# Performance work log

Measured on AMD Instinct MI355X. Metric: run time of the kernel, lower is better.

The kernel has to match this reference:

```python
import jax, jax.numpy as jnp
import numpy as np

D = 1024
H = 16
HD = D // H
T = 2048
B = 2
EPS = 1e-7

def setup_inputs() -> dict:
    key = jax.random.key(0)
    ks = jax.random.split(key, 16)
    s = 0.02
    return {
        "x":  jax.random.normal(ks[0], (B, T, D), jnp.float32),
        "Wq": jax.random.normal(ks[1], (D, D), jnp.float32) * s,
        "bq": jnp.zeros((D,), jnp.float32),
        "Wk": jax.random.normal(ks[2], (D, D), jnp.float32) * s,
        "bk": jnp.zeros((D,), jnp.float32),
        "Wv": jax.random.normal(ks[3], (D, D), jnp.float32) * s,
        "bv": jnp.zeros((D,), jnp.float32),
        "Wo": jax.random.normal(ks[4], (D, D), jnp.float32) * s,
        "bo": jnp.zeros((D,), jnp.float32),
        "W1": jax.random.normal(ks[5], (D, 4 * D), jnp.float32) * s,
        "b1": jnp.zeros((4 * D,), jnp.float32),
        "W2": jax.random.normal(ks[6], (4 * D, D), jnp.float32) * s,
        "b2": jnp.zeros((D,), jnp.float32),
        "g1": jnp.ones((D,), jnp.float32),
        "be1": jnp.zeros((D,), jnp.float32),
        "g2": jnp.ones((D,), jnp.float32),
        "be2": jnp.zeros((D,), jnp.float32),
    }

def layer_norm(x, gamma, beta):
    mu = jnp.mean(x, axis=-1, keepdims=True)
    var = jnp.mean(jnp.square(x - mu), axis=-1, keepdims=True)  # biased var
    return (x - mu) / jnp.sqrt(var + EPS) * gamma + beta

def attention(x, Wq, bq, Wk, bk, Wv, bv, Wo, bo):
    b, t, d = x.shape
    q = (x @ Wq + bq).reshape(b, t, H, HD).transpose(0, 2, 1, 3)  # [B,H,T,HD]
    k = (x @ Wk + bk).reshape(b, t, H, HD).transpose(0, 2, 1, 3)
    v = (x @ Wv + bv).reshape(b, t, H, HD).transpose(0, 2, 1, 3)
    scores = jnp.einsum("bhqd,bhkd->bhqk", q, k) / np.sqrt(HD).astype(np.float32)
    causal = jnp.tril(jnp.ones((t, t), bool))
    scores = jnp.where(causal, scores, -jnp.inf)
    attn = jax.nn.softmax(scores, axis=-1)
    out = jnp.einsum("bhqk,bhkd->bhqd", attn, v)
    out = out.transpose(0, 2, 1, 3).reshape(b, t, d)
    return out @ Wo + bo

def reference(x, Wq, bq, Wk, bk, Wv, bv, Wo, bo, W1, b1, W2, b2, g1, be1, g2, be2):
    x = x + attention(layer_norm(x, g1, be1), Wq, bq, Wk, bk, Wv, bv, Wo, bo)
    h = layer_norm(x, g2, be2)
    x = x + (jax.nn.relu(h @ W1 + b1) @ W2 + b2)
    return x
```

## Files before the change

kernel.cpp:

```cpp
#include <hip/hip_runtime.h>
#include <hip/hip_bf16.h>

#define Dm 1024
#define Hn 16
#define HDm 64
#define Tm 2048
#define Bm 2
#define MR (Bm*Tm)
#define SQK 3072

typedef __attribute__((ext_vector_type(8))) short bfrag8;
typedef __attribute__((ext_vector_type(4))) float floatx4;

__device__ __forceinline__ float bf2f(ushort u){
  union { unsigned int i; float f; } c; c.i = ((unsigned int)u)<<16; return c.f;
}
__device__ __forceinline__ ushort f2bf(float f){
  unsigned int u = __float_as_uint(f);
  u += 0x7fffu + ((u>>16)&1u);
  return (ushort)(u>>16);
}
__device__ __forceinline__ void gl2lds16(const ushort* g, ushort* l){
  __builtin_amdgcn_global_load_lds(
    (const __attribute__((address_space(1))) unsigned int*)g,
    (__attribute__((address_space(3))) unsigned int*)l,
    16, 0, 0);
}
__device__ __forceinline__ int is_f32(const unsigned int* g1w){
  return *g1w == 0x3F800000u;
}

#define POFF0 (1ul*524288)
#define POFF1 (9ul*524288)
#define POFF2 (25ul*524288)
#define POFF3 (73ul*524288)

__global__ __launch_bounds__(256) void prep_vec(const void* bq, const void* bk, const void* bv,
                                                const void* bo, const void* b1, const void* b2,
                                                const void* g1, const void* be1,
                                                const void* g2, const void* be2,
                                                float* __restrict__ dst){
  int i = blockIdx.x*256 + threadIdx.x;
  if (i >= 13312) return;
  int f = is_f32((const unsigned int*)g1);
  const void* src; int off;
  if      (i < 1024)  { src = bq;  off = i; }
  else if (i < 2048)  { src = bk;  off = i-1024; }
  else if (i < 3072)  { src = bv;  off = i-2048; }
  else if (i < 4096)  { src = bo;  off = i-3072; }
  else if (i < 8192)  { src = b1;  off = i-4096; }
  else if (i < 9216)  { src = b2;  off = i-8192; }
  else if (i < 10240) { src = g1;  off = i-9216; }
  else if (i < 11264) { src = be1; off = i-10240; }
  else if (i < 12288) { src = g2;  off = i-11264; }
  else                { src = be2; off = i-12288; }
  dst[i] = f ? ((const float*)src)[off] : bf2f(((const ushort*)src)[off]);
}

__device__ __forceinline__ void transpose_body(const void* src, ushort* dst,
                                               int K, int N, int f32){
  __shared__ ushort s[32][33];
  int bx = blockIdx.x, by = blockIdx.y;
  int tx = threadIdx.x, ty = threadIdx.y;
#pragma unroll
  for(int r=0;r<4;r++){
    size_t gi = (size_t)(by*32+ty+8*r)*N + bx*32+tx;
    s[ty+8*r][tx] = f32 ? f2bf(((const float*)src)[gi]) : ((const ushort*)src)[gi];
  }
  __syncthreads();
#pragma unroll
  for(int r=0;r<4;r++)
    dst[(size_t)(bx*32+ty+8*r)*K + by*32+tx] = s[tx][ty+8*r];
}
__global__ __launch_bounds__(256) void transpose_cast(const void* __restrict__ src,
                                                      ushort* __restrict__ dst,
                                                      int K, int N, const unsigned int* g1w){
  transpose_body(src, dst, K, N, is_f32(g1w));
}
__global__ __launch_bounds__(256) void transpose_qkvo(const void* Wq, const void* Wk,
                                                      const void* Wv, const void* Wo,
                                                      ushort* __restrict__ Wqkvt,
                                                      ushort* __restrict__ Wot,
                                                      const unsigned int* g1w){
  int z = blockIdx.z;
  const void* src = (z==0)?Wq:(z==1)?Wk:(z==2)?Wv:Wo;
  ushort* dst = (z<3) ? (Wqkvt + (size_t)z*1024*1024) : Wot;
  transpose_body(src, dst, 1024, 1024, is_f32(g1w));
}

__global__ __launch_bounds__(256) void vtrans(const ushort* __restrict__ qkv,
                                              ushort* __restrict__ vt){
  __shared__ ushort s[32][33];
  int bhz = blockIdx.z;
  int bx = blockIdx.x;
  int by = blockIdx.y;
  int tx = threadIdx.x, ty = threadIdx.y;
  int b = bhz>>4, h = bhz&15;
  const ushort* src = qkv + (size_t)b*Tm*SQK + 2048 + h*64;
#pragma unroll
  for(int r=0;r<4;r++)
    s[ty+8*r][tx] = src[(size_t)(bx*32+ty+8*r)*SQK + by*32+tx];
  __syncthreads();
  ushort* dst = vt + (size_t)bhz*HDm*Tm;
#pragma unroll
  for(int r=0;r<4;r++)
    dst[(size_t)(by*32+ty+8*r)*Tm + bx*32+tx] = s[tx][ty+8*r];
}

template<int MODE>
__global__ __launch_bounds__(256) void ln_kernel(const void* __restrict__ xin,
                                                 const float* __restrict__ g,
                                                 const float* __restrict__ be,
                                                 ushort* __restrict__ out,
                                                 const unsigned int* g1w){
  int row = blockIdx.x;
  int tid = threadIdx.x;
  size_t base = (size_t)row*Dm + tid*4;
  float v[4];
  bool f32in = (MODE==1) || (MODE==0 && is_f32(g1w));
  if (f32in){
    const float4 t = *(const float4*)((const float*)xin + base);
    v[0]=t.x; v[1]=t.y; v[2]=t.z; v[3]=t.w;
  } else {
    ushort4 t = *(const ushort4*)((const ushort*)xin + base);
    v[0]=bf2f(t.x); v[1]=bf2f(t.y); v[2]=bf2f(t.z); v[3]=bf2f(t.w);
  }
  float s  = v[0]+v[1]+v[2]+v[3];
  float s2 = v[0]*v[0]+v[1]*v[1]+v[2]*v[2]+v[3]*v[3];
#pragma unroll
  for(int o=1;o<64;o<<=1){
    s  += __shfl_xor(s,  o, 64);
    s2 += __shfl_xor(s2, o, 64);
  }
  __shared__ float red[8];
  int wv = tid>>6;
  if ((tid&63)==0){ red[wv]=s; red[wv+4]=s2; }
  __syncthreads();
  s  = red[0]+red[1]+red[2]+red[3];
  s2 = red[4]+red[5]+red[6]+red[7];
  float mu  = s  * (1.0f/Dm);
  float var = s2 * (1.0f/Dm) - mu*mu;
  float rstd = rsqrtf(var + 1e-7f);
  float4 gg = *(const float4*)(g  + tid*4);
  float4 bb = *(const float4*)(be + tid*4);
  ushort4 o4;
  o4.x = f2bf((v[0]-mu)*rstd*gg.x+bb.x);
  o4.y = f2bf((v[1]-mu)*rstd*gg.y+bb.y);
  o4.z = f2bf((v[2]-mu)*rstd*gg.z+bb.z);
  o4.w = f2bf((v[3]-mu)*rstd*gg.w+bb.w);
  *(ushort4*)(out + base) = o4;
}

#define BKt 64
enum { E_BF16=0, E_RELU=1, E_OPROJ=2, E_FINALB=3, E_PARTB=4, E_PARTB4=5 };

template<int EPI>
__global__ __launch_bounds__(512,2) void gemm256(const ushort* __restrict__ A, int lda,
                                                 const ushort* __restrict__ Bt, int ldb,
                                                 const float* __restrict__ bias,
                                                 void* __restrict__ Cout, int ldc,
                                                 int Ki,
                                                 const unsigned int* g1w){
  __shared__ ushort lds[65536];
  int tid = threadIdx.x;
  int lin = blockIdx.x;
  int xcd = lin&7, pos = lin>>3;
  int bm, bn, zid = 0;
  if (EPI==E_BF16){        bm=(xcd&3)*4+(pos&3);  bn=(xcd>>2)*6+(pos>>2); }
  else if (EPI==E_RELU){   bm=(xcd&3)*4+(pos&3);  bn=(xcd>>2)*8+(pos>>2); }
  else if (EPI==E_PARTB4){ zid=xcd>>1; bm=(xcd&1)*8+(pos>>2); bn=pos&3; }
  else {                   zid=xcd&1;  bm=(xcd>>1)*4+(pos>>2); bn=pos&3; }
  int wv = tid>>6, lane = tid&63;
  int quad = lane>>4, l16 = lane&15;
  int wm = (wv>>2)*128, wn = (wv&3)*64;
  int rl = lane>>3;
  int cs = ((lane&7)^rl)*8;
  const ushort* Aptr = A  + (size_t)bm*256*lda + (size_t)zid*Ki;
  const ushort* Bptr = Bt + (size_t)bn*256*ldb + (size_t)zid*Ki;
  floatx4 acc[8][4] = {};
  bfrag8 afr[4][2], bfr[4][2];
  const int NI = Ki>>7;

  auto STG = [&](ushort* dst, const ushort* g, int ld){
    gl2lds16(&g[(size_t)(wv*16+rl)*ld + cs],   dst + (wv*16)*64);
    gl2lds16(&g[(size_t)(wv*16+8+rl)*ld + cs], dst + (wv*16+8)*64);
  };
  auto LD8 = [&](const ushort* base, int r, int G)->bfrag8{
    return *(const bfrag8*)&base[r*64 + ((G ^ (r&7))<<3)];
  };
#define BAR256 __builtin_amdgcn_s_barrier()
#define LGKM0  do{ asm volatile("s_waitcnt lgkmcnt(0)" ::: "memory"); __builtin_amdgcn_sched_barrier(0);}while(0)
#define MM256(a_,b_,c_) c_ = __builtin_amdgcn_mfma_f32_16x16x32_bf16(a_,b_,c_,0,0,0)

  STG(lds+32768,      Bptr,                    ldb);
  STG(lds+32768+8192, Bptr+(size_t)128*ldb,    ldb);
  STG(lds,            Aptr,                    lda);
  STG(lds+8192,       Aptr+(size_t)128*lda,    lda);
  STG(lds+49152,      Bptr+64,                 ldb);
  STG(lds+49152+8192, Bptr+(size_t)128*ldb+64, ldb);
  STG(lds+16384,      Aptr+64,                 lda);
  asm volatile("s_waitcnt vmcnt(6)" ::: "memory");
  BAR256;

  for(int i=0;i<NI;i++){
    bool nl = (i < NI-1);
    int kc = i*128;
#pragma unroll
    for(int m=0;m<4;m++){ int r=wm+m*16+l16;
      afr[m][0]=LD8(lds, r, quad);  afr[m][1]=LD8(lds, r, 4|quad); }
#pragma unroll
    for(int j=0;j<4;j++){ int r=wn+j*16+l16;
      bfr[j][0]=LD8(lds+32768, r, quad); bfr[j][1]=LD8(lds+32768, r, 4|quad); }
    STG(lds+16384+8192, Aptr+(size_t)128*lda + kc+64, lda);
    BAR256; LGKM0;
    __builtin_amdgcn_s_setprio(1);
#pragma unroll
    for(int m=0;m<4;m++)
#pragma unroll
      for(int j=0;j<2;j++){ MM256(afr[m][0],bfr[j][0],acc[m][j]); MM256(afr[m][1],bfr[j][1],acc[m][j]); }
    __builtin_amdgcn_s_setprio(0);
    BAR256;
    if(nl) STG(lds+32768, Bptr + kc+128, ldb);
    BAR256;
    __builtin_amdgcn_s_setprio(1);
#pragma unroll
    for(int m=0;m<4;m++)
#pragma unroll
      for(int j=2;j<4;j++){ MM256(afr[m][0],bfr[j][0],acc[m][j]); MM256(afr[m][1],bfr[j][1],acc[m][j]); }
    __builtin_amdgcn_s_setprio(0);
    BAR256;
#pragma unroll
    for(int m=0;m<4;m++){ int r=wm+(4+m)*16+l16;
      afr[m][0]=LD8(lds, r, quad);  afr[m][1]=LD8(lds, r, 4|quad); }
    if(nl) STG(lds+32768+8192, Bptr+(size_t)128*ldb + kc+128, ldb);
    BAR256; LGKM0;
    __builtin_amdgcn_s_setprio(1);
#pragma unroll
    for(int m=0;m<4;m++)
#pragma unroll
      for(int j=2;j<4;j++){ MM256(afr[m][0],bfr[j][0],acc[4+m][j]); MM256(afr[m][1],bfr[j][1],acc[4+m][j]); }
    __builtin_amdgcn_s_setprio(0);
    BAR256;
    if(nl) STG(lds, Aptr + kc+128, lda);
    BAR256;
    __builtin_amdgcn_s_setprio(1);
#pragma unroll
    for(int m=0;m<4;m++)
#pragma unroll
      for(int j=0;j<2;j++){ MM256(afr[m][0],bfr[j][0],acc[4+m][j]); MM256(afr[m][1],bfr[j][1],acc[4+m][j]); }
    __builtin_amdgcn_s_setprio(0);
    if(nl) asm volatile("s_waitcnt vmcnt(6)" ::: "memory");
    else   asm volatile("s_waitcnt vmcnt(0)" ::: "memory");
    BAR256;
#pragma unroll
    for(int m=0;m<4;m++){ int r=wm+m*16+l16;
      afr[m][0]=LD8(lds+16384, r, quad);  afr[m][1]=LD8(lds+16384, r, 4|quad); }
#pragma unroll
    for(int j=0;j<4;j++){ int r=wn+j*16+l16;
      bfr[j][0]=LD8(lds+49152, r, quad); bfr[j][1]=LD8(lds+49152, r, 4|quad); }
    if(nl) STG(lds+8192, Aptr+(size_t)128*lda + kc+128, lda);
    BAR256; LGKM0;
    __builtin_amdgcn_s_setprio(1);
#pragma unroll
    for(int m=0;m<4;m++)
#pragma unroll
      for(int j=0;j<2;j++){ MM256(afr[m][0],bfr[j][0],acc[m][j]); MM256(afr[m][1],bfr[j][1],acc[m][j]); }
    __builtin_amdgcn_s_setprio(0);
    BAR256;
    if(nl) STG(lds+49152, Bptr + kc+192, ldb);
    BAR256;
    __builtin_amdgcn_s_setprio(1);
#pragma unroll
    for(int m=0;m<4;m++)
#pragma unroll
      for(int j=2;j<4;j++){ MM256(afr[m][0],bfr[j][0],acc[m][j]); MM256(afr[m][1],bfr[j][1],acc[m][j]); }
    __builtin_amdgcn_s_setprio(0);
    BAR256;
#pragma unroll
    for(int m=0;m<4;m++){ int r=wm+(4+m)*16+l16;
      afr[m][0]=LD8(lds+16384, r, quad);  afr[m][1]=LD8(lds+16384, r, 4|quad); }
    if(nl) STG(lds+49152+8192, Bptr+(size_t)128*ldb + kc+192, ldb);
    BAR256; LGKM0;
    __builtin_amdgcn_s_setprio(1);
#pragma unroll
    for(int m=0;m<4;m++)
#pragma unroll
      for(int j=2;j<4;j++){ MM256(afr[m][0],bfr[j][0],acc[4+m][j]); MM256(afr[m][1],bfr[j][1],acc[4+m][j]); }
    __builtin_amdgcn_s_setprio(0);
    BAR256;
    if(nl) STG(lds+16384, Aptr + kc+192, lda);
    BAR256;
    __builtin_amdgcn_s_setprio(1);
#pragma unroll
    for(int m=0;m<4;m++)
#pragma unroll
      for(int j=0;j<2;j++){ MM256(afr[m][0],bfr[j][0],acc[4+m][j]); MM256(afr[m][1],bfr[j][1],acc[4+m][j]); }
    __builtin_amdgcn_s_setprio(0);
    if(nl){ asm volatile("s_waitcnt vmcnt(6)" ::: "memory"); }
    BAR256;
  }

  ushort* part = (ushort*)Cout;
  if (EPI==E_PARTB)  part += (size_t)zid*MR*1024;
  if (EPI==E_PARTB4) part += (zid==0?POFF0 : zid==1?POFF1 : zid==2?POFF2 : POFF3);
#pragma unroll
  for(int i2=0;i2<8;i2++){
    int gr = bm*256 + wm + i2*16 + quad*4;
#pragma unroll
    for(int j=0;j<4;j++){
      int gc = bn*256 + wn + j*16 + l16;
      float bb = (EPI==E_PARTB || EPI==E_PARTB4) ? 0.0f : bias[gc];
#pragma unroll
      for(int rg=0; rg<4; rg++){
        size_t idx = (size_t)(gr+rg)*ldc + gc;
        float val = acc[i2][j][rg] + bb;
        if (EPI==E_RELU) part[idx] = f2bf(val>0.0f?val:0.0f);
        else             part[idx] = f2bf(val);
      }
    }
  }
#undef BAR256
#undef LGKM0
#undef MM256
}

__global__ __launch_bounds__(256) void ffn2_reduce(const ushort* __restrict__ p0,
                                                   const ushort* __restrict__ p1,
                                                   const float* __restrict__ bias,
                                                   const ushort* __restrict__ resid,
                                                   void* __restrict__ out,
                                                   const unsigned int* g1w){
  int e = (blockIdx.x*256 + threadIdx.x)*4;
  ushort4 a = *(const ushort4*)&p0[e];
  ushort4 b = *(const ushort4*)&p1[e];
  ushort4 r = *(const ushort4*)&resid[e];
  float4 bb = *(const float4*)&bias[e & 1023];
  float v0 = bf2f(a.x)+bf2f(b.x)+bb.x+bf2f(r.x);
  float v1 = bf2f(a.y)+bf2f(b.y)+bb.y+bf2f(r.y);
  float v2 = bf2f(a.z)+bf2f(b.z)+bb.z+bf2f(r.z);
  float v3 = bf2f(a.w)+bf2f(b.w)+bb.w+bf2f(r.w);
  if (is_f32(g1w)){
    float4 o = {v0,v1,v2,v3};
    *(float4*)((float*)out + e) = o;
  } else {
    ushort4 o = {f2bf(v0),f2bf(v1),f2bf(v2),f2bf(v3)};
    *(ushort4*)((ushort*)out + e) = o;
  }
}

__global__ __launch_bounds__(256) void ffn2_reduce4(const ushort* __restrict__ pb,
                                                    const float* __restrict__ bias,
                                                    const ushort* __restrict__ resid,
                                                    void* __restrict__ out,
                                                    const unsigned int* g1w){
  int e = (blockIdx.x*256 + threadIdx.x)*4;
  ushort4 a = *(const ushort4*)&pb[POFF0 + e];
  ushort4 b = *(const ushort4*)&pb[POFF1 + e];
  ushort4 c = *(const ushort4*)&pb[POFF2 + e];
  ushort4 d = *(const ushort4*)&pb[POFF3 + e];
  ushort4 r = *(const ushort4*)&resid[e];
  float4 bb = *(const float4*)&bias[e & 1023];
  float v0 = bf2f(a.x)+bf2f(b.x)+bf2f(c.x)+bf2f(d.x)+bb.x+bf2f(r.x);
  float v1 = bf2f(a.y)+bf2f(b.y)+bf2f(c.y)+bf2f(d.y)+bb.y+bf2f(r.y);
  float v2 = bf2f(a.z)+bf2f(b.z)+bf2f(c.z)+bf2f(d.z)+bb.z+bf2f(r.z);
  float v3 = bf2f(a.w)+bf2f(b.w)+bf2f(c.w)+bf2f(d.w)+bb.w+bf2f(r.w);
  if (is_f32(g1w)){
    float4 o = {v0,v1,v2,v3};
    *(float4*)((float*)out + e) = o;
  } else {
    ushort4 o = {f2bf(v0),f2bf(v1),f2bf(v2),f2bf(v3)};
    *(ushort4*)((ushort*)out + e) = o;
  }
}

template<int EPI>
__global__ __launch_bounds__(128) void gemm64_bt(const ushort* __restrict__ A, int lda,
                                                 const ushort* __restrict__ Bt, int ldb,
                                                 const float* __restrict__ bias,
                                                 const void*   __restrict__ resid,
                                                 void* __restrict__ Cout, int ldc,
                                                 int Ki,
                                                 const unsigned int* g1w){
  __shared__ ushort As[64*BKt];
  __shared__ ushort Bs[64*BKt];
  int tid = threadIdx.x;
  int id = blockIdx.x;
  int xcd = id&7, sdec = id>>3;
  int bn = sdec&15, bm = (sdec>>4)*8 + xcd;
  int wv = tid>>6, lane = tid&63;
  int quad = lane>>4, l16 = lane&15;
  int wm = wv*32;
  floatx4 acc[2][4] = {};
  const ushort* Aptr = A  + (size_t)bm*64*lda;
  const ushort* Bptr = Bt + (size_t)bn*64*ldb;
  int rl = lane>>3;
  int cs = ((lane&7) ^ rl)*8;

  for(int k0=0; k0<Ki; k0+=BKt){
    __syncthreads();
#pragma unroll
    for(int c=0;c<4;c++){
      gl2lds16(&Aptr[(size_t)(wv*32 + c*8 + rl)*lda + k0 + cs], &As[(wv*32 + c*8)*BKt]);
      gl2lds16(&Bptr[(size_t)(wv*32 + c*8 + rl)*ldb + k0 + cs], &Bs[(wv*32 + c*8)*BKt]);
    }
    __syncthreads();
#pragma unroll
    for(int f=0;f<2;f++){
      int sw = (((f<<2)|quad) ^ (l16&7))*8;
      bfrag8 a[2], b[4];
#pragma unroll
      for(int i=0;i<2;i++) a[i] = *(const bfrag8*)&As[(wm+i*16+l16)*BKt + sw];
#pragma unroll
      for(int j=0;j<4;j++) b[j] = *(const bfrag8*)&Bs[(j*16+l16)*BKt + sw];
#pragma unroll
      for(int i=0;i<2;i++)
#pragma unroll
        for(int j=0;j<4;j++)
          acc[i][j] = __builtin_amdgcn_mfma_f32_16x16x32_bf16(a[i], b[j], acc[i][j], 0,0,0);
    }
  }

  int f32 = is_f32(g1w);
#pragma unroll
  for(int i=0;i<2;i++){
    int gr = bm*64 + wm + i*16 + quad*4;
#pragma unroll
    for(int j=0;j<4;j++){
      int gc = bn*64 + j*16 + l16;
      float bb = bias[gc];
#pragma unroll
      for(int rg=0; rg<4; rg++){
        size_t idx = (size_t)(gr+rg)*ldc + gc;
        float val = acc[i][j][rg] + bb;
        if (EPI==E_OPROJ){
          float r = f32 ? ((const float*)resid)[idx] : bf2f(((const ushort*)resid)[idx]);
          ((ushort*)Cout)[idx] = f2bf(val + r);
        } else {
          float r = bf2f(((const ushort*)resid)[idx]);
          if (f32) ((float*)Cout)[idx] = val + r;
          else     ((ushort*)Cout)[idx] = f2bf(val + r);
        }
      }
    }
  }
}

#define PSTR2 132

__global__ __launch_bounds__(256) void attn_mfma(const ushort* __restrict__ qkv,
                                                 const ushort* __restrict__ vt,
                                                 ushort* __restrict__ out){
  __shared__ ushort Ks[128*64];
  __shared__ ushort Vs[64*128];
  __shared__ ushort Ps[64*PSTR2];
  int id = blockIdx.x;
  int xcd = id&7, sdec = id>>3;
  int qt = 31 - (sdec&31);
  int hb = sdec>>5;
  int h = xcd + 8*(hb&1), b = hb>>1;
  int tid = threadIdx.x;
  int wv = tid>>6, lane = tid&63;
  int quad = lane>>4, l16 = lane&15;
  const ushort* qbase = qkv + (size_t)b*Tm*SQK + h*HDm;
  const ushort* kbase = qbase + Dm;
  const ushort* vtb   = vt + (size_t)(b*Hn+h)*HDm*Tm;
  size_t obase = (size_t)b*Tm*Dm + (size_t)h*HDm;
  int rl = lane>>3;
  int cs = ((lane&7) ^ rl)*8;
  int vrow = lane>>4;
  int vg = lane&15;

  int qrow = qt*64 + wv*16 + l16;
  bfrag8 aq[2];
#pragma unroll
  for(int f=0;f<2;f++){
    bfrag8 raw = *(const bfrag8*)&qbase[(size_t)qrow*SQK + f*32 + quad*8];
#pragma unroll
    for(int e=0;e<8;e++) aq[f][e] = (short)f2bf(bf2f((ushort)raw[e])*0.125f);
  }

  floatx4 oacc[4] = {};
  float lacc = 0.0f;
  int qglob = qt*64 + wv*16 + l16;
  int nr = (qt+2)>>1;

  for(int r=0; r<nr; r++){
    __syncthreads();
#pragma unroll
    for(int c=0;c<4;c++){
      int kr0 = wv*32 + c*8;
      gl2lds16(&kbase[(size_t)(r*128 + kr0 + rl)*SQK + cs], &Ks[kr0*64]);
      int d0 = wv*16 + c*4;
      int drow = d0 + vrow;
      int gg = vg ^ (drow&7);
      gl2lds16(&vtb[(size_t)drow*Tm + r*128 + gg*8], &Vs[d0*128]);
    }
    __syncthreads();

    floatx4 s[8];
#pragma unroll
    for(int j=0;j<8;j++){
      int kr = j*16 + l16;
      int k7 = kr & 7;
      bfrag8 k0 = *(const bfrag8*)&Ks[kr*64 + ((quad     ^ k7)*8)];
      bfrag8 k1 = *(const bfrag8*)&Ks[kr*64 + (((4|quad) ^ k7)*8)];
      floatx4 z = {0.0f,0.0f,0.0f,0.0f};
      z = __builtin_amdgcn_mfma_f32_16x16x32_bf16(k0, aq[0], z, 0,0,0);
      z = __builtin_amdgcn_mfma_f32_16x16x32_bf16(k1, aq[1], z, 0,0,0);
      s[j] = z;
    }
    if (2*r+1 >= qt){
#pragma unroll
      for(int j=0;j<8;j++){
        int gk0 = r*128 + j*16 + quad*4;
#pragma unroll
        for(int rg=0;rg<4;rg++)
          if (gk0 + rg > qglob) s[j][rg] = -1.0e30f;
      }
    }

#pragma unroll
    for(int j=0;j<8;j++){
      float p0 = __expf(s[j][0]);
      float p1 = __expf(s[j][1]);
      float p2 = __expf(s[j][2]);
      float p3 = __expf(s[j][3]);
      lacc += (p0+p1)+(p2+p3);
      unsigned w0, w1;
      asm("v_cvt_pk_bf16_f32 %0, %1, %2" : "=v"(w0) : "v"(p0), "v"(p1));
      asm("v_cvt_pk_bf16_f32 %0, %1, %2" : "=v"(w1) : "v"(p2), "v"(p3));
      uint2 ww; ww.x = w0; ww.y = w1;
      *(uint2*)&Ps[(wv*16 + l16)*PSTR2 + j*16 + quad*4] = ww;
    }

    bfrag8 ap[4];
#pragma unroll
    for(int c=0;c<4;c++)
      ap[c] = *(const bfrag8*)&Ps[(wv*16 + l16)*PSTR2 + c*32 + quad*8];

#pragma unroll
    for(int j=0;j<4;j++){
      int dr = j*16 + l16;
      int d7 = dr & 7;
#pragma unroll
      for(int c=0;c<4;c++){
        bfrag8 bv = *(const bfrag8*)&Vs[dr*128 + (((c*4+quad) ^ d7)*8)];
        oacc[j] = __builtin_amdgcn_mfma_f32_16x16x32_bf16(ap[c], bv, oacc[j], 0,0,0);
      }
    }
  }

  lacc += __shfl_xor(lacc, 16, 64);
  lacc += __shfl_xor(lacc, 32, 64);
  float inv[4];
#pragma unroll
  for(int rg=0;rg<4;rg++){
    float den = __shfl(lacc, quad*4 + rg, 64);
    inv[rg] = 1.0f / den;
  }

#pragma unroll
  for(int j=0;j<4;j++)
#pragma unroll
    for(int rg=0;rg<4;rg++){
      int t = qt*64 + wv*16 + quad*4 + rg;
      out[obase + (size_t)t*Dm + j*16 + l16] = f2bf(oacc[j][rg] * inv[rg]);
    }
}

extern "C" void kernel_launch(void* const* d_in, const int* in_sizes, int n_in,
                              void* d_out, int out_size, void* d_ws, size_t ws_size,
                              hipStream_t stream) {
  const void* x   = d_in[0];
  const void* Wq  = d_in[1];
  const void* bq  = d_in[2];
  const void* Wk  = d_in[3];
  const void* bk  = d_in[4];
  const void* Wv  = d_in[5];
  const void* bv  = d_in[6];
  const void* Wo  = d_in[7];
  const void* bo  = d_in[8];
  const void* W1  = d_in[9];
  const void* b1  = d_in[10];
  const void* W2  = d_in[11];
  const void* b2  = d_in[12];
  const void* g1  = d_in[13];
  const void* be1 = d_in[14];
  const void* g2  = d_in[15];
  const void* be2 = d_in[16];
  const unsigned int* g1w = (const unsigned int*)g1;

  char* ws = (char*)d_ws;
  const size_t MB = 1024*1024;
  float*  biasf = (float*)(ws + 65536);
  ushort* Wqkvt = (ushort*)(ws + 1*MB);
  ushort* Wot   = (ushort*)(ws + 7*MB);
  ushort* W1t   = (ushort*)(ws + 9*MB);
  ushort* W2t   = (ushort*)(ws + 17*MB);
  ushort* p0    = (ushort*)(ws + 1*MB);
  ushort* p1    = (ushort*)(ws + 9*MB);
  ushort* ln1   = (ushort*)(ws + 25*MB);
  ushort* vtb   = (ushort*)(ws + 25*MB);
  ushort* h2    = (ushort*)(ws + 25*MB);
  ushort* qkv   = (ushort*)(ws + 33*MB);
  ushort* atb   = (ushort*)(ws + 57*MB);
  ushort* x1b   = (ushort*)(ws + 65*MB);
  ushort* h1    = (ushort*)(ws + 33*MB);

  prep_vec<<<52, 256, 0, stream>>>(bq,bk,bv,bo,b1,b2,g1,be1,g2,be2, biasf);

  dim3 tb(32,8);
  transpose_qkvo<<<dim3(32,32,4), tb, 0, stream>>>(Wq, Wk, Wv, Wo, Wqkvt, Wot, g1w);
  transpose_cast<<<dim3(128,32), tb, 0, stream>>>(W1, W1t, 1024, 4096, g1w);
  transpose_cast<<<dim3(32,128), tb, 0, stream>>>(W2, W2t, 4096, 1024, g1w);

  ln_kernel<0><<<MR, 256, 0, stream>>>(x, biasf+9216, biasf+10240, ln1, g1w);

  gemm256<E_BF16><<<192, 512, 0, stream>>>(ln1, 1024, Wqkvt, 1024, biasf, qkv, SQK, 1024, g1w);

  vtrans<<<dim3(64,2,32), tb, 0, stream>>>(qkv, vtb);

  attn_mfma<<<1024, 256, 0, stream>>>(qkv, vtb, atb);

  gemm64_bt<E_OPROJ><<<1024, 128, 0, stream>>>(atb, 1024, Wot, 1024, biasf+3072, x, x1b, 1024, 1024, g1w);

  ln_kernel<2><<<MR, 256, 0, stream>>>(x1b, biasf+11264, biasf+12288, h2, g1w);

  gemm256<E_RELU><<<256, 512, 0, stream>>>(h2, 1024, W1t, 1024, biasf+4096, h1, 4096, 1024, g1w);

  if (ws_size >= 82*MB){
    gemm256<E_PARTB4><<<256, 512, 0, stream>>>(h1, 4096, W2t, 4096, nullptr, d_ws, 1024, 1024, g1w);
    ffn2_reduce4<<<4096, 256, 0, stream>>>((const ushort*)d_ws, biasf+8192, x1b, d_out, g1w);
  } else {
    gemm256<E_PARTB><<<128, 512, 0, stream>>>(h1, 4096, W2t, 4096, nullptr, p0, 1024, 2048, g1w);
    ffn2_reduce<<<4096, 256, 0, stream>>>(p0, p1, biasf+8192, x1b, d_out, g1w);
  }
}
```

Before: 339.8 us.

## Halve attention block to two waves, each processing two 16-row query groups

The attention kernel now runs 128 threads per block instead of 256. Each wave handles 32 query rows as two 16-row groups, so every K and V fragment read from LDS feeds two MFMAs. Each wave issues twice as many global-to-LDS loads per tile, and the P buffer stride changes from 132 to 136. The aim is fewer LDS reads per MFMA, at the cost of more registers per wave and fewer waves per block to hide latency.

```diff
diff --git a/kernel.cpp b/kernel.cpp
--- a/kernel.cpp
+++ b/kernel.cpp
@@ -445,9 +445,9 @@
   }
 }
 
-#define PSTR2 132
-
-__global__ __launch_bounds__(256) void attn_mfma(const ushort* __restrict__ qkv,
+#define PSTR2 136
+
+__global__ __launch_bounds__(128) void attn_mfma(const ushort* __restrict__ qkv,
                                                  const ushort* __restrict__ vt,
                                                  ushort* __restrict__ out){
   __shared__ ushort Ks[128*64];
@@ -470,73 +470,87 @@
   int vrow = lane>>4;
   int vg = lane&15;
 
-  int qrow = qt*64 + wv*16 + l16;
-  bfrag8 aq[2];
-#pragma unroll
-  for(int f=0;f<2;f++){
-    bfrag8 raw = *(const bfrag8*)&qbase[(size_t)qrow*SQK + f*32 + quad*8];
-#pragma unroll
-    for(int e=0;e<8;e++) aq[f][e] = (short)f2bf(bf2f((ushort)raw[e])*0.125f);
-  }
-
-  floatx4 oacc[4] = {};
-  float lacc = 0.0f;
-  int qglob = qt*64 + wv*16 + l16;
+  bfrag8 aq[2][2];
+#pragma unroll
+  for(int g=0;g<2;g++){
+    int qrow = qt*64 + wv*32 + g*16 + l16;
+#pragma unroll
+    for(int f=0;f<2;f++){
+      bfrag8 raw = *(const bfrag8*)&qbase[(size_t)qrow*SQK + f*32 + quad*8];
+#pragma unroll
+      for(int e=0;e<8;e++) aq[g][f][e] = (short)f2bf(bf2f((ushort)raw[e])*0.125f);
+    }
+  }
+
+  floatx4 oacc[2][4] = {};
+  float lacc[2] = {0.0f, 0.0f};
   int nr = (qt+2)>>1;
 
   for(int r=0; r<nr; r++){
     __syncthreads();
 #pragma unroll
-    for(int c=0;c<4;c++){
-      int kr0 = wv*32 + c*8;
+    for(int c=0;c<8;c++){
+      int kr0 = wv*64 + c*8;
       gl2lds16(&kbase[(size_t)(r*128 + kr0 + rl)*SQK + cs], &Ks[kr0*64]);
-      int d0 = wv*16 + c*4;
+      int d0 = wv*32 + c*4;
       int drow = d0 + vrow;
       int gg = vg ^ (drow&7);
       gl2lds16(&vtb[(size_t)drow*Tm + r*128 + gg*8], &Vs[d0*128]);
     }
     __syncthreads();
 
-    floatx4 s[8];
+    floatx4 s[2][8];
 #pragma unroll
     for(int j=0;j<8;j++){
       int kr = j*16 + l16;
       int k7 = kr & 7;
       bfrag8 k0 = *(const bfrag8*)&Ks[kr*64 + ((quad     ^ k7)*8)];
       bfrag8 k1 = *(const bfrag8*)&Ks[kr*64 + (((4|quad) ^ k7)*8)];
-      floatx4 z = {0.0f,0.0f,0.0f,0.0f};
-      z = __builtin_amdgcn_mfma_f32_16x16x32_bf16(k0, aq[0], z, 0,0,0);
-      z = __builtin_amdgcn_mfma_f32_16x16x32_bf16(k1, aq[1], z, 0,0,0);
-      s[j] = z;
+#pragma unroll
+      for(int g=0;g<2;g++){
+        floatx4 z = {0.0f,0.0f,0.0f,0.0f};
+        z = __builtin_amdgcn_mfma_f32_16x16x32_bf16(k0, aq[g][0], z, 0,0,0);
+        z = __builtin_amdgcn_mfma_f32_16x16x32_bf16(k1, aq[g][1], z, 0,0,0);
+        s[g][j] = z;
+      }
     }
     if (2*r+1 >= qt){
 #pragma unroll
+      for(int g=0;g<2;g++){
+        int qg = qt*64 + wv*32 + g*16 + l16;
+#pragma unroll
+        for(int j=0;j<8;j++){
+          int gk0 = r*128 + j*16 + quad*4;
+#pragma unroll
+          for(int rg=0;rg<4;rg++)
+            if (gk0 + rg > qg) s[g][j][rg] = -1.0e30f;
+        }
+      }
+    }
+
+#pragma unroll
+    for(int g=0;g<2;g++){
+#pragma unroll
       for(int j=0;j<8;j++){
-        int gk0 = r*128 + j*16 + quad*4;
-#pragma unroll
-        for(int rg=0;rg<4;rg++)
-          if (gk0 + rg > qglob) s[j][rg] = -1.0e30f;
+        float p0 = __expf(s[g][j][0]);
+        float p1 = __expf(s[g][j][1]);
+        float p2 = __expf(s[g][j][2]);
+        float p3 = __expf(s[g][j][3]);
+        lacc[g] += (p0+p1)+(p2+p3);
+        unsigned w0, w1;
+        asm("v_cvt_pk_bf16_f32 %0, %1, %2" : "=v"(w0) : "v"(p0), "v"(p1));
+        asm("v_cvt_pk_bf16_f32 %0, %1, %2" : "=v"(w1) : "v"(p2), "v"(p3));
+        uint2 ww; ww.x = w0; ww.y = w1;
+        *(uint2*)&Ps[(wv*32 + g*16 + l16)*PSTR2 + j*16 + quad*4] = ww;
       }
     }
 
-#pragma unroll
-    for(int j=0;j<8;j++){
-      float p0 = __expf(s[j][0]);
-      float p1 = __expf(s[j][1]);
-      float p2 = __expf(s[j][2]);
-      float p3 = __expf(s[j][3]);
-      lacc += (p0+p1)+(p2+p3);
-      unsigned w0, w1;
-      asm("v_cvt_pk_bf16_f32 %0, %1, %2" : "=v"(w0) : "v"(p0), "v"(p1));
-      asm("v_cvt_pk_bf16_f32 %0, %1, %2" : "=v"(w1) : "v"(p2), "v"(p3));
-      uint2 ww; ww.x = w0; ww.y = w1;
-      *(uint2*)&Ps[(wv*16 + l16)*PSTR2 + j*16 + quad*4] = ww;
-    }
-
-    bfrag8 ap[4];
-#pragma unroll
-    for(int c=0;c<4;c++)
-      ap[c] = *(const bfrag8*)&Ps[(wv*16 + l16)*PSTR2 + c*32 + quad*8];
+    bfrag8 ap[2][4];
+#pragma unroll
+    for(int g=0;g<2;g++)
+#pragma unroll
+      for(int c=0;c<4;c++)
+        ap[g][c] = *(const bfrag8*)&Ps[(wv*32 + g*16 + l16)*PSTR2 + c*32 + quad*8];
 
 #pragma unroll
     for(int j=0;j<4;j++){
@@ -545,27 +559,34 @@
 #pragma unroll
       for(int c=0;c<4;c++){
         bfrag8 bv = *(const bfrag8*)&Vs[dr*128 + (((c*4+quad) ^ d7)*8)];
-        oacc[j] = __builtin_amdgcn_mfma_f32_16x16x32_bf16(ap[c], bv, oacc[j], 0,0,0);
+#pragma unroll
+        for(int g=0;g<2;g++)
+          oacc[g][j] = __builtin_amdgcn_mfma_f32_16x16x32_bf16(ap[g][c], bv, oacc[g][j], 0,0,0);
       }
     }
   }
 
-  lacc += __shfl_xor(lacc, 16, 64);
-  lacc += __shfl_xor(lacc, 32, 64);
-  float inv[4];
-#pragma unroll
-  for(int rg=0;rg<4;rg++){
-    float den = __shfl(lacc, quad*4 + rg, 64);
-    inv[rg] = 1.0f / den;
-  }
-
-#pragma unroll
-  for(int j=0;j<4;j++)
+#pragma unroll
+  for(int g=0;g<2;g++){
+    lacc[g] += __shfl_xor(lacc[g], 16, 64);
+    lacc[g] += __shfl_xor(lacc[g], 32, 64);
+  }
+#pragma unroll
+  for(int g=0;g<2;g++){
+    float inv[4];
 #pragma unroll
     for(int rg=0;rg<4;rg++){
-      int t = qt*64 + wv*16 + quad*4 + rg;
-      out[obase + (size_t)t*Dm + j*16 + l16] = f2bf(oacc[j][rg] * inv[rg]);
-    }
+      float den = __shfl(lacc[g], quad*4 + rg, 64);
+      inv[rg] = 1.0f / den;
+    }
+#pragma unroll
+    for(int j=0;j<4;j++)
+#pragma unroll
+      for(int rg=0;rg<4;rg++){
+        int t = qt*64 + wv*32 + g*16 + quad*4 + rg;
+        out[obase + (size_t)t*Dm + j*16 + l16] = f2bf(oacc[g][j][rg] * inv[rg]);
+      }
+  }
 }
 
 extern "C" void kernel_launch(void* const* d_in, const int* in_sizes, int n_in,
@@ -620,7 +641,7 @@
 
   vtrans<<<dim3(64,2,32), tb, 0, stream>>>(qkv, vtb);
 
-  attn_mfma<<<1024, 256, 0, stream>>>(qkv, vtb, atb);
+  attn_mfma<<<1024, 128, 0, stream>>>(qkv, vtb, atb);
 
   gemm64_bt<E_OPROJ><<<1024, 128, 0, stream>>>(atb, 1024, Wot, 1024, biasf+3072, x, x1b, 1024, 1024, g1w);
 
```

Measured after the change: 350.0 us. 3.0% more time.

## Shrink attention KV tile to 64 keys and balance causal work across blocks

Applied to the files above, without the earlier changes.

The causal attention kernel now processes 64 keys per iteration instead of 128. This halves the LDS footprint and skips less masked work on the diagonal, since only the last tile needs masking. Block-to-query-tile mapping now alternates forward and reverse order between head halves, so blocks sharing a CU get complementary amounts of causal work. The trade-off is twice as many loop iterations, each with its own barrier pair and load issue.

```diff
diff --git a/kernel.cpp b/kernel.cpp
--- a/kernel.cpp
+++ b/kernel.cpp
@@ -445,19 +445,19 @@
   }
 }
 
-#define PSTR2 132
+#define PSTR2 72
 
 __global__ __launch_bounds__(256) void attn_mfma(const ushort* __restrict__ qkv,
                                                  const ushort* __restrict__ vt,
                                                  ushort* __restrict__ out){
-  __shared__ ushort Ks[128*64];
-  __shared__ ushort Vs[64*128];
+  __shared__ ushort Ks[64*64];
+  __shared__ ushort Vs[64*64];
   __shared__ ushort Ps[64*PSTR2];
   int id = blockIdx.x;
-  int xcd = id&7, sdec = id>>3;
-  int qt = 31 - (sdec&31);
-  int hb = sdec>>5;
-  int h = xcd + 8*(hb&1), b = hb>>1;
+  int xcd = id&7, s = id>>3;
+  int cu = s&31, k = s>>5;
+  int qt = (k&1) ? cu : 31-cu;
+  int h = xcd + 8*(k&1), b = k>>1;
   int tid = threadIdx.x;
   int wv = tid>>6, lane = tid&63;
   int quad = lane>>4, l16 = lane&15;
@@ -467,8 +467,6 @@
   size_t obase = (size_t)b*Tm*Dm + (size_t)h*HDm;
   int rl = lane>>3;
   int cs = ((lane&7) ^ rl)*8;
-  int vrow = lane>>4;
-  int vg = lane&15;
 
   int qrow = qt*64 + wv*16 + l16;
   bfrag8 aq[2];
@@ -482,24 +480,21 @@
   floatx4 oacc[4] = {};
   float lacc = 0.0f;
   int qglob = qt*64 + wv*16 + l16;
-  int nr = (qt+2)>>1;
+  int nr = qt + 1;
 
   for(int r=0; r<nr; r++){
     __syncthreads();
 #pragma unroll
-    for(int c=0;c<4;c++){
-      int kr0 = wv*32 + c*8;
-      gl2lds16(&kbase[(size_t)(r*128 + kr0 + rl)*SQK + cs], &Ks[kr0*64]);
-      int d0 = wv*16 + c*4;
-      int drow = d0 + vrow;
-      int gg = vg ^ (drow&7);
-      gl2lds16(&vtb[(size_t)drow*Tm + r*128 + gg*8], &Vs[d0*128]);
+    for(int c=0;c<2;c++){
+      int kr0 = wv*16 + c*8;
+      gl2lds16(&kbase[(size_t)(r*64 + kr0 + rl)*SQK + cs], &Ks[kr0*64]);
+      gl2lds16(&vtb[(size_t)(kr0 + rl)*Tm + r*64 + cs], &Vs[kr0*64]);
     }
     __syncthreads();
 
-    floatx4 s[8];
-#pragma unroll
-    for(int j=0;j<8;j++){
+    floatx4 sv[4];
+#pragma unroll
+    for(int j=0;j<4;j++){
       int kr = j*16 + l16;
       int k7 = kr & 7;
       bfrag8 k0 = *(const bfrag8*)&Ks[kr*64 + ((quad     ^ k7)*8)];
@@ -507,24 +502,24 @@
       floatx4 z = {0.0f,0.0f,0.0f,0.0f};
       z = __builtin_amdgcn_mfma_f32_16x16x32_bf16(k0, aq[0], z, 0,0,0);
       z = __builtin_amdgcn_mfma_f32_16x16x32_bf16(k1, aq[1], z, 0,0,0);
-      s[j] = z;
-    }
-    if (2*r+1 >= qt){
-#pragma unroll
-      for(int j=0;j<8;j++){
-        int gk0 = r*128 + j*16 + quad*4;
+      sv[j] = z;
+    }
+    if (r == qt){
+#pragma unroll
+      for(int j=0;j<4;j++){
+        int gk0 = r*64 + j*16 + quad*4;
 #pragma unroll
         for(int rg=0;rg<4;rg++)
-          if (gk0 + rg > qglob) s[j][rg] = -1.0e30f;
+          if (gk0 + rg > qglob) sv[j][rg] = -1.0e30f;
       }
     }
 
 #pragma unroll
-    for(int j=0;j<8;j++){
-      float p0 = __expf(s[j][0]);
-      float p1 = __expf(s[j][1]);
-      float p2 = __expf(s[j][2]);
-      float p3 = __expf(s[j][3]);
+    for(int j=0;j<4;j++){
+      float p0 = __expf(sv[j][0]);
+      float p1 = __expf(sv[j][1]);
+      float p2 = __expf(sv[j][2]);
+      float p3 = __expf(sv[j][3]);
       lacc += (p0+p1)+(p2+p3);
       unsigned w0, w1;
       asm("v_cvt_pk_bf16_f32 %0, %1, %2" : "=v"(w0) : "v"(p0), "v"(p1));
@@ -533,9 +528,9 @@
       *(uint2*)&Ps[(wv*16 + l16)*PSTR2 + j*16 + quad*4] = ww;
     }
 
-    bfrag8 ap[4];
-#pragma unroll
-    for(int c=0;c<4;c++)
+    bfrag8 ap[2];
+#pragma unroll
+    for(int c=0;c<2;c++)
       ap[c] = *(const bfrag8*)&Ps[(wv*16 + l16)*PSTR2 + c*32 + quad*8];
 
 #pragma unroll
@@ -543,8 +538,8 @@
       int dr = j*16 + l16;
       int d7 = dr & 7;
 #pragma unroll
-      for(int c=0;c<4;c++){
-        bfrag8 bv = *(const bfrag8*)&Vs[dr*128 + (((c*4+quad) ^ d7)*8)];
+      for(int c=0;c<2;c++){
+        bfrag8 bv = *(const bfrag8*)&Vs[dr*64 + (((c*4+quad) ^ d7)*8)];
         oacc[j] = __builtin_amdgcn_mfma_f32_16x16x32_bf16(ap[c], bv, oacc[j], 0,0,0);
       }
     }
```

Measured after the change: 336.5 us. About the same (-1.0%).
